# Performance work log

Measured on AMD Instinct MI355X. Metric: run time of the kernel, lower is better.

The kernel has to match this reference:

```python
import jax, jax.numpy as jnp
import numpy as np
import math

S = 30.0
M = 0.5
COS_M = math.cos(M)
SIN_M = math.sin(M)
TH = math.cos(math.pi - M)
MM = math.sin(math.pi - M) * M
B, D, C = 512, 512, 100000


def setup_inputs() -> dict:
    key = jax.random.key(0)
    k1, k2, k3 = jax.random.split(key, 3)
    inp = jax.random.normal(k1, (B, D), dtype=jnp.float32)
    weight = jax.random.normal(k2, (C, D), dtype=jnp.float32) * (1.0 / math.sqrt(D))
    label = jax.random.randint(k3, (B,), 0, C, dtype=jnp.int64)
    return {"input": inp, "label": label, "weight": weight}


def _l2norm(x, axis=-1, eps=1e-12):
    # matches F.normalize: x / max(||x||, eps)
    n = jnp.sqrt(jnp.sum(x * x, axis=axis, keepdims=True))
    return x / jnp.maximum(n, eps)


def reference(input, label, weight):
    # cosine: [B, C]
    cosine = jnp.clip(_l2norm(input) @ _l2norm(weight).T, -1.0, 1.0)
    sine = jnp.sqrt(jnp.clip(1.0 - cosine * cosine, 1e-9, 1.0))
    phi = cosine * COS_M - sine * SIN_M
    phi = jnp.where(cosine > TH, phi, cosine - MM)  # easy_margin=False branch
    one_hot = (label[:, None] == jnp.arange(cosine.shape[1])[None, :])
    out = jnp.where(one_hot, phi, cosine) * S
    return out
```

## Files before the change

kernel.cpp:

```cpp
#include <hip/hip_runtime.h>
#include <hip/hip_bf16.h>

#define ARC_S    30.0f
#define ARC_COSM 0.8775825618903728f
#define ARC_SINM 0.4794255386042030f
#define ARC_TH  -0.8775825618903728f
#define ARC_MM   0.2397127693021015f

#define B_ROWS 512
#define D_DIM  512
#define C_CLS  100000
#define C_PAD  100096

typedef float  floatx4 __attribute__((ext_vector_type(4)));
typedef __bf16 bf16x8  __attribute__((ext_vector_type(8)));

__global__ __launch_bounds__(256) void normalize_rows_512(
    const float* __restrict__ src, __bf16* __restrict__ dst, int valid_rows)
{
    const int lane = threadIdx.x & 63;
    const int wave = threadIdx.x >> 6;
    const long long row = (long long)blockIdx.x * 4 + wave;

    __bf16* drow = dst + row * D_DIM;

    if (row >= valid_rows) {
        bf16x8 z;
        #pragma unroll
        for (int i = 0; i < 8; i++) z[i] = (__bf16)0.0f;
        *(bf16x8*)(drow + lane * 8) = z;
        return;
    }

    const float4* rp = (const float4*)(src + row * D_DIM);
    float4 p0 = rp[lane * 2];
    float4 p1 = rp[lane * 2 + 1];

    float ss = p0.x*p0.x + p0.y*p0.y + p0.z*p0.z + p0.w*p0.w
             + p1.x*p1.x + p1.y*p1.y + p1.z*p1.z + p1.w*p1.w;
    #pragma unroll
    for (int m = 32; m >= 1; m >>= 1) ss += __shfl_xor(ss, m, 64);

    const float scale = 1.0f / fmaxf(sqrtf(ss), 1e-12f);

    bf16x8 v;
    v[0] = (__bf16)(p0.x * scale);
    v[1] = (__bf16)(p0.y * scale);
    v[2] = (__bf16)(p0.z * scale);
    v[3] = (__bf16)(p0.w * scale);
    v[4] = (__bf16)(p1.x * scale);
    v[5] = (__bf16)(p1.y * scale);
    v[6] = (__bf16)(p1.z * scale);
    v[7] = (__bf16)(p1.w * scale);
    *(bf16x8*)(drow + lane * 8) = v;
}

#define BM 256
#define BN 128
#define BK 32
#define KSTEPS  (D_DIM / BK)
#define N_TILES 782
#define GRID_B  1568

#define WAITVM(N) asm volatile("s_waitcnt vmcnt(" #N ")" ::: "memory")
#define BARRIER() asm volatile("s_barrier" ::: "memory")

__device__ inline void async_load_16B(__bf16* lds, const __bf16* gmem)
{
    __builtin_amdgcn_global_load_lds(
        (const __attribute__((address_space(1))) void*)gmem,
        (__attribute__((address_space(3))) void*)lds,
        16, 0, 0);
}

__global__ __launch_bounds__(512, 4) void gemm_arcface(
    const __bf16* __restrict__ A,
    const __bf16* __restrict__ W,
    const int*    __restrict__ label,
    float*        __restrict__ out)
{
    const int b  = blockIdx.x;
    const int nt = (b & 7) + 8 * (b >> 4);
    const int mt = (b >> 3) & 1;
    if (nt >= N_TILES) return;

    __shared__ __bf16 As[2][BM * BK];
    __shared__ __bf16 Bs[3][BN * BK];
    __shared__ int    sLab[BM];

    const int tid = threadIdx.x;
    const int m0  = mt * BM;
    const int n0  = nt * BN;

    if (tid < BM) sLab[tid] = label[m0 + tid];

    const int lane = tid & 63;
    const int wave = tid >> 6;
    const int wr   = wave >> 1;
    const int wc   = wave & 1;
    const int frow = lane & 15;
    const int fch  = lane >> 4;

    const int srow = tid >> 2;
    const int skc  = (tid & 3) ^ ((tid >> 3) & 3);

    const __bf16* gA0 = A + (long long)(m0 + srow) * D_DIM + skc * 8;
    const __bf16* gA1 = gA0 + (long long)128 * D_DIM;
    const __bf16* gB0 = W + (long long)(n0 + srow) * D_DIM + skc * 8;

    int aoff[4], boff[4];
    #pragma unroll
    for (int i = 0; i < 4; i++) {
        const int ar = wr * 64 + i * 16 + frow;
        aoff[i] = ar * BK + ((fch ^ ((ar >> 1) & 3)) << 3);
        const int br = wc * 64 + i * 16 + frow;
        boff[i] = br * BK + ((fch ^ ((br >> 1) & 3)) << 3);
    }

    floatx4 acc[4][4];
    #pragma unroll
    for (int i = 0; i < 4; i++)
        #pragma unroll
        for (int j = 0; j < 4; j++)
            acc[i][j] = (floatx4)(0.0f);

    async_load_16B(&As[0][tid * 8],         gA0);
    async_load_16B(&As[0][(tid + 512) * 8], gA1);
    async_load_16B(&Bs[0][tid * 8],         gB0);
    async_load_16B(&Bs[1][tid * 8],         gB0 + BK);

    #pragma unroll
    for (int t = 0; t < KSTEPS; ++t) {
        if (t + 1 < KSTEPS) {
            const int u = t + 1;
            async_load_16B(&As[u & 1][tid * 8],         gA0 + u * BK);
            async_load_16B(&As[u & 1][(tid + 512) * 8], gA1 + u * BK);
        }
        if (t + 2 < KSTEPS) {
            const int u = t + 2;
            async_load_16B(&Bs[u % 3][tid * 8],         gB0 + u * BK);
        }

        if (t <= KSTEPS - 3)      WAITVM(4);
        else if (t == KSTEPS - 2) WAITVM(3);
        else                      WAITVM(0);
        BARRIER();

        const __bf16* as = &As[t & 1][0];
        const __bf16* bs = &Bs[t % 3][0];
        bf16x8 a[4], bb[4];
        #pragma unroll
        for (int i = 0; i < 4; i++) a[i]  = *(const bf16x8*)(as + aoff[i]);
        #pragma unroll
        for (int j = 0; j < 4; j++) bb[j] = *(const bf16x8*)(bs + boff[j]);

        __builtin_amdgcn_s_setprio(1);
        #pragma unroll
        for (int i = 0; i < 4; i++)
            #pragma unroll
            for (int j = 0; j < 4; j++)
                acc[i][j] = __builtin_amdgcn_mfma_f32_16x16x32_bf16(
                    a[i], bb[j], acc[i][j], 0, 0, 0);
        __builtin_amdgcn_s_setprio(0);

        if (t + 1 < KSTEPS) BARRIER();
    }

    const int mrow = (lane >> 4) * 4;
    const int ncol = lane & 15;

    #pragma unroll
    for (int i = 0; i < 4; i++) {
        #pragma unroll
        for (int r = 0; r < 4; r++) {
            const int ml  = wr * 64 + i * 16 + mrow + r;
            const int m   = m0 + ml;
            const int lab = sLab[ml];
            float* orow = out + (long long)m * C_CLS;
            #pragma unroll
            for (int j = 0; j < 4; j++) {
                const int cls = n0 + wc * 64 + j * 16 + ncol;
                if (cls < C_CLS) {
                    float c = fminf(fmaxf(acc[i][j][r], -1.0f), 1.0f);
                    float o = c * ARC_S;
                    if (lab == cls) {
                        float tt  = fminf(fmaxf(1.0f - c * c, 1e-9f), 1.0f);
                        float s   = sqrtf(tt);
                        float phi = c * ARC_COSM - s * ARC_SINM;
                        phi = (c > ARC_TH) ? phi : (c - ARC_MM);
                        o = phi * ARC_S;
                    }
                    orow[cls] = o;
                }
            }
        }
    }
}

extern "C" void kernel_launch(void* const* d_in, const int* in_sizes, int n_in,
                              void* d_out, int out_size, void* d_ws, size_t ws_size,
                              hipStream_t stream)
{
    const float* inp    = (const float*)d_in[0];
    const int*   label  = (const int*)d_in[1];
    const float* weight = (const float*)d_in[2];
    float*       out    = (float*)d_out;

    __bf16* A = (__bf16*)d_ws;
    __bf16* W = A + (size_t)B_ROWS * D_DIM;

    normalize_rows_512<<<B_ROWS / 4, 256, 0, stream>>>(inp, A, B_ROWS);
    normalize_rows_512<<<C_PAD / 4, 256, 0, stream>>>(weight, W, C_CLS);
    gemm_arcface<<<GRID_B, 512, 0, stream>>>(A, W, label, out);
}
```

Baseline: 430.4 us.

## Enlarge GEMM tile to 256x256x64 with quadrant-phased MFMA schedule and nontemporal stores

Switches the GEMM tile from 256x128 with BK=32 to 256x256 with BK=64, halving the grid and using a 2x4 wave layout. Each K step is split into four quadrant phases that interleave LDS fragment loads, async global-to-LDS staging and MFMAs, with an 8-way XOR swizzle and double buffering. Output stores become nontemporal. The goal is more data reuse per loaded byte and less traffic for the 205 MB output. The cost is fewer blocks, lower occupancy and extra barriers per phase.

```diff
diff --git a/kernel.cpp b/kernel.cpp
--- a/kernel.cpp
+++ b/kernel.cpp
@@ -56,13 +56,14 @@
 }
 
 #define BM 256
-#define BN 128
-#define BK 32
-#define KSTEPS  (D_DIM / BK)
-#define N_TILES 782
-#define GRID_B  1568
+#define BN 256
+#define BK 64
+#define KT 8
+#define N_TILES 391
+#define GRID_B  784
 
 #define WAITVM(N) asm volatile("s_waitcnt vmcnt(" #N ")" ::: "memory")
+#define WAITLG0() asm volatile("s_waitcnt lgkmcnt(0)" ::: "memory")
 #define BARRIER() asm volatile("s_barrier" ::: "memory")
 
 __device__ inline void async_load_16B(__bf16* lds, const __bf16* gmem)
@@ -73,7 +74,7 @@
         16, 0, 0);
 }
 
-__global__ __launch_bounds__(512, 4) void gemm_arcface(
+__global__ __launch_bounds__(512, 2) void gemm_arcface(
     const __bf16* __restrict__ A,
     const __bf16* __restrict__ W,
     const int*    __restrict__ label,
@@ -85,7 +86,7 @@
     if (nt >= N_TILES) return;
 
     __shared__ __bf16 As[2][BM * BK];
-    __shared__ __bf16 Bs[3][BN * BK];
+    __shared__ __bf16 Bs[2][BN * BK];
     __shared__ int    sLab[BM];
 
     const int tid = threadIdx.x;
@@ -96,105 +97,146 @@
 
     const int lane = tid & 63;
     const int wave = tid >> 6;
-    const int wr   = wave >> 1;
-    const int wc   = wave & 1;
+    const int wr   = wave >> 2;
+    const int wc   = wave & 3;
     const int frow = lane & 15;
     const int fch  = lane >> 4;
 
-    const int srow = tid >> 2;
-    const int skc  = (tid & 3) ^ ((tid >> 3) & 3);
-
-    const __bf16* gA0 = A + (long long)(m0 + srow) * D_DIM + skc * 8;
-    const __bf16* gA1 = gA0 + (long long)128 * D_DIM;
-    const __bf16* gB0 = W + (long long)(n0 + srow) * D_DIM + skc * 8;
-
-    int aoff[4], boff[4];
-    #pragma unroll
-    for (int i = 0; i < 4; i++) {
-        const int ar = wr * 64 + i * 16 + frow;
-        aoff[i] = ar * BK + ((fch ^ ((ar >> 1) & 3)) << 3);
-        const int br = wc * 64 + i * 16 + frow;
-        boff[i] = br * BK + ((fch ^ ((br >> 1) & 3)) << 3);
+    const int lrow = tid >> 3;
+    const int kcs  = (tid & 7) ^ (lrow & 7);
+    const __bf16* pA0 = A + (long long)(m0 + lrow) * D_DIM + kcs * 8;
+    const __bf16* pB0 = W + (long long)(n0 + lrow) * D_DIM + kcs * 8;
+    const __bf16* pA1 = pA0 + 128 * D_DIM;
+    const __bf16* pB1 = pB0 + 128 * D_DIM;
+
+    #define STAGE(k, h) do {                                                  \
+        const __bf16* _g = ((h) == 0 ? pA0 : (h) == 1 ? pB0 :                 \
+                            (h) == 2 ? pB1 : pA1) + (k) * BK;                 \
+        __bf16* _l = (((h) == 0 || (h) == 3) ? &As[(k) & 1][0]                \
+                                             : &Bs[(k) & 1][0])               \
+                     + (((h) >= 2) ? 128 * BK : 0);                           \
+        async_load_16B(_l + tid * 8,         _g);                             \
+        async_load_16B(_l + (tid + 512) * 8, _g + 64 * D_DIM);                \
+    } while (0)
+
+    int aoff[4][2], boff[2][2];
+    #pragma unroll
+    for (int ks = 0; ks < 2; ks++) {
+        const int col = ((ks * 4 + fch) ^ (frow & 7)) * 8;
+        #pragma unroll
+        for (int mi = 0; mi < 4; mi++) aoff[mi][ks] = (mi * 16 + frow) * BK + col;
+        #pragma unroll
+        for (int nj = 0; nj < 2; nj++) boff[nj][ks] = (nj * 16 + frow) * BK + col;
     }
-
-    floatx4 acc[4][4];
-    #pragma unroll
-    for (int i = 0; i < 4; i++)
-        #pragma unroll
-        for (int j = 0; j < 4; j++)
-            acc[i][j] = (floatx4)(0.0f);
-
-    async_load_16B(&As[0][tid * 8],         gA0);
-    async_load_16B(&As[0][(tid + 512) * 8], gA1);
-    async_load_16B(&Bs[0][tid * 8],         gB0);
-    async_load_16B(&Bs[1][tid * 8],         gB0 + BK);
-
-    #pragma unroll
-    for (int t = 0; t < KSTEPS; ++t) {
-        if (t + 1 < KSTEPS) {
-            const int u = t + 1;
-            async_load_16B(&As[u & 1][tid * 8],         gA0 + u * BK);
-            async_load_16B(&As[u & 1][(tid + 512) * 8], gA1 + u * BK);
+    const int aW = wr * 64 * BK;
+    const int bW = wc * 32 * BK;
+
+    floatx4 acc[2][4][2][2];
+    #pragma unroll
+    for (int mh = 0; mh < 2; mh++)
+        #pragma unroll
+        for (int mi = 0; mi < 4; mi++)
+            #pragma unroll
+            for (int nh = 0; nh < 2; nh++)
+                #pragma unroll
+                for (int nj = 0; nj < 2; nj++)
+                    acc[mh][mi][nh][nj] = (floatx4)(0.0f);
+
+    bf16x8 a[4][2], b0[2][2], b1[2][2];
+
+    STAGE(0, 0); STAGE(0, 1); STAGE(0, 2); STAGE(0, 3);
+    STAGE(1, 0); STAGE(1, 1); STAGE(1, 2); STAGE(1, 3);
+
+    #pragma unroll
+    for (int p = 0; p < 4 * KT; ++p) {
+        const int g = p >> 2;
+        const int q = p & 3;
+
+        if (p >= 1 && p <= 24) { const int e = p - 1; STAGE(2 + (e >> 2), e & 3); }
+
+        if (q == 0) {
+            if (g < KT - 1) WAITVM(8);
+            else            WAITVM(0);
         }
-        if (t + 2 < KSTEPS) {
-            const int u = t + 2;
-            async_load_16B(&Bs[u % 3][tid * 8],         gB0 + u * BK);
+        BARRIER();
+
+        const __bf16* as = &As[g & 1][0];
+        const __bf16* bs = &Bs[g & 1][0];
+        if (q == 0) {
+            #pragma unroll
+            for (int mi = 0; mi < 4; mi++)
+                #pragma unroll
+                for (int ks = 0; ks < 2; ks++)
+                    a[mi][ks] = *(const bf16x8*)(as + aW + aoff[mi][ks]);
+            #pragma unroll
+            for (int nj = 0; nj < 2; nj++)
+                #pragma unroll
+                for (int ks = 0; ks < 2; ks++)
+                    b0[nj][ks] = *(const bf16x8*)(bs + bW + boff[nj][ks]);
+        } else if (q == 1) {
+            #pragma unroll
+            for (int nj = 0; nj < 2; nj++)
+                #pragma unroll
+                for (int ks = 0; ks < 2; ks++)
+                    b1[nj][ks] = *(const bf16x8*)(bs + 128 * BK + bW + boff[nj][ks]);
+        } else if (q == 2) {
+            #pragma unroll
+            for (int mi = 0; mi < 4; mi++)
+                #pragma unroll
+                for (int ks = 0; ks < 2; ks++)
+                    a[mi][ks] = *(const bf16x8*)(as + 128 * BK + aW + aoff[mi][ks]);
         }
 
-        if (t <= KSTEPS - 3)      WAITVM(4);
-        else if (t == KSTEPS - 2) WAITVM(3);
-        else                      WAITVM(0);
+        WAITLG0();
+        __builtin_amdgcn_sched_barrier(0);
+
+        const int mh = q >> 1;
+        const int nh = (q == 1 || q == 2) ? 1 : 0;
+        __builtin_amdgcn_s_setprio(1);
+        #pragma unroll
+        for (int mi = 0; mi < 4; mi++)
+            #pragma unroll
+            for (int nj = 0; nj < 2; nj++)
+                #pragma unroll
+                for (int ks = 0; ks < 2; ks++)
+                    acc[mh][mi][nh][nj] = __builtin_amdgcn_mfma_f32_16x16x32_bf16(
+                        a[mi][ks], (nh ? b1 : b0)[nj][ks], acc[mh][mi][nh][nj], 0, 0, 0);
+        __builtin_amdgcn_s_setprio(0);
         BARRIER();
-
-        const __bf16* as = &As[t & 1][0];
-        const __bf16* bs = &Bs[t % 3][0];
-        bf16x8 a[4], bb[4];
-        #pragma unroll
-        for (int i = 0; i < 4; i++) a[i]  = *(const bf16x8*)(as + aoff[i]);
-        #pragma unroll
-        for (int j = 0; j < 4; j++) bb[j] = *(const bf16x8*)(bs + boff[j]);
-
-        __builtin_amdgcn_s_setprio(1);
-        #pragma unroll
-        for (int i = 0; i < 4; i++)
-            #pragma unroll
-            for (int j = 0; j < 4; j++)
-                acc[i][j] = __builtin_amdgcn_mfma_f32_16x16x32_bf16(
-                    a[i], bb[j], acc[i][j], 0, 0, 0);
-        __builtin_amdgcn_s_setprio(0);
-
-        if (t + 1 < KSTEPS) BARRIER();
     }
+    #undef STAGE
 
     const int mrow = (lane >> 4) * 4;
     const int ncol = lane & 15;
 
     #pragma unroll
-    for (int i = 0; i < 4; i++) {
-        #pragma unroll
-        for (int r = 0; r < 4; r++) {
-            const int ml  = wr * 64 + i * 16 + mrow + r;
-            const int m   = m0 + ml;
-            const int lab = sLab[ml];
-            float* orow = out + (long long)m * C_CLS;
-            #pragma unroll
-            for (int j = 0; j < 4; j++) {
-                const int cls = n0 + wc * 64 + j * 16 + ncol;
-                if (cls < C_CLS) {
-                    float c = fminf(fmaxf(acc[i][j][r], -1.0f), 1.0f);
-                    float o = c * ARC_S;
-                    if (lab == cls) {
-                        float tt  = fminf(fmaxf(1.0f - c * c, 1e-9f), 1.0f);
-                        float s   = sqrtf(tt);
-                        float phi = c * ARC_COSM - s * ARC_SINM;
-                        phi = (c > ARC_TH) ? phi : (c - ARC_MM);
-                        o = phi * ARC_S;
+    for (int mh = 0; mh < 2; mh++)
+        #pragma unroll
+        for (int mi = 0; mi < 4; mi++)
+            #pragma unroll
+            for (int r = 0; r < 4; r++) {
+                const int ml  = wr * 64 + mh * 128 + mi * 16 + mrow + r;
+                const int lab = sLab[ml];
+                float* orow = out + (long long)(m0 + ml) * C_CLS;
+                #pragma unroll
+                for (int nh = 0; nh < 2; nh++)
+                    #pragma unroll
+                    for (int nj = 0; nj < 2; nj++) {
+                        const int cls = n0 + wc * 32 + nh * 128 + nj * 16 + ncol;
+                        if (cls < C_CLS) {
+                            float c = fminf(fmaxf(acc[mh][mi][nh][nj][r], -1.0f), 1.0f);
+                            float o = c * ARC_S;
+                            if (lab == cls) {
+                                float tt  = fminf(fmaxf(1.0f - c * c, 1e-9f), 1.0f);
+                                float s   = sqrtf(tt);
+                                float phi = c * ARC_COSM - s * ARC_SINM;
+                                phi = (c > ARC_TH) ? phi : (c - ARC_MM);
+                                o = phi * ARC_S;
+                            }
+                            __builtin_nontemporal_store(o, &orow[cls]);
+                        }
                     }
-                    orow[cls] = o;
-                }
             }
-        }
-    }
 }
 
 extern "C" void kernel_launch(void* const* d_in, const int* in_sizes, int n_in,
```

Result: no change. 434.0 us (+0.8%).
